# Performance work log

Hardware: AMD Instinct MI355X
Metric: run time of the kernel (lower is better)

Reference implementation:

```python
import jax, jax.numpy as jnp
import numpy as np

N_GRAPHS = 5000
NODES_PER_GRAPH = 100
EDGES_PER_GRAPH = 400
N_NODES = N_GRAPHS * NODES_PER_GRAPH
N_EDGES = N_GRAPHS * EDGES_PER_GRAPH
K = 2
DIMS = [74, 70, 65, 60, 55, 37]


def setup_inputs() -> dict:
    key = jax.random.key(0)
    ks = jax.random.split(key, 16)
    x = jax.random.normal(ks[0], (N_NODES, DIMS[0]), dtype=jnp.float32)
    # edges constrained within each graph: base node offset per graph + random local node
    edge_base = (jnp.arange(N_EDGES, dtype=jnp.int32) // EDGES_PER_GRAPH) * NODES_PER_GRAPH
    src = edge_base + jax.random.randint(ks[1], (N_EDGES,), 0, NODES_PER_GRAPH, dtype=jnp.int32)
    dst = edge_base + jax.random.randint(ks[2], (N_EDGES,), 0, NODES_PER_GRAPH, dtype=jnp.int32)
    graph_ids = (jnp.arange(N_NODES, dtype=jnp.int32) // NODES_PER_GRAPH)
    inp = {"x": x, "src": src, "dst": dst, "graph_ids": graph_ids}
    # TAGConv weights: Linear(in*(K+1) -> out) + bias, for each of 5 layers
    for i in range(5):
        fan_in = DIMS[i] * (K + 1)
        w = jax.random.normal(ks[3 + 2 * i], (fan_in, DIMS[i + 1]), dtype=jnp.float32) / np.sqrt(fan_in)
        b = jnp.zeros((DIMS[i + 1],), dtype=jnp.float32)
        inp[f"W{i}"] = w
        inp[f"b{i}"] = b
    inp["gate_w"] = jax.random.normal(ks[13], (DIMS[-1], 1), dtype=jnp.float32) / np.sqrt(DIMS[-1])
    inp["gate_b"] = jnp.zeros((1,), dtype=jnp.float32)
    return inp


def _forward(x, src, dst, graph_ids, Ws, bs, gate_w, gate_b):
    n = x.shape[0]
    # symmetric normalization with in-degree (DGL TAGConv convention), clamp min 1
    deg = jax.ops.segment_sum(jnp.ones_like(src, dtype=x.dtype), dst, num_segments=n)
    norm = jnp.clip(deg, 1.0, None) ** -0.5  # [N]
    norm = norm[:, None]

    def tagconv(h, W, b):
        feats = [h]
        cur = h
        for _ in range(K):
            msg = (cur * norm)[src]  # gather over edges
            cur = norm * jax.ops.segment_sum(msg, dst, num_segments=n)
            feats.append(cur)
        return jnp.concatenate(feats, axis=-1) @ W + b

    h = x
    for W, b in zip(Ws, bs):
        h = jax.nn.relu(tagconv(h, W, b))

    # GlobalAttentionPooling: per-graph softmax over gate scores, weighted sum
    gate = (h @ gate_w + gate_b)[:, 0]  # [N]
    gmax = jax.ops.segment_max(gate, graph_ids, num_segments=N_GRAPHS)
    e = jnp.exp(gate - gmax[graph_ids])
    z = jax.ops.segment_sum(e, graph_ids, num_segments=N_GRAPHS)
    alpha = e / z[graph_ids]
    pooled = jax.ops.segment_sum(h * alpha[:, None], graph_ids, num_segments=N_GRAPHS)  # [G, 37]
    return pooled.reshape(-1, 2, DIMS[-1])


def reference(x, src, dst, graph_ids, W0, b0, W1, b1, W2, b2, W3, b3, W4, b4, gate_w, gate_b):
    Ws = [W0, W1, W2, W3, W4]
    bs = [b0, b1, b2, b3, b4]
    return _forward(x, src, dst, graph_ids, Ws, bs, gate_w, gate_b)
```

## Files before the change

### kernel.cpp

```cpp
#include <hip/hip_runtime.h>
#include <math.h>


typedef __attribute__((ext_vector_type(8))) short bf16x8;
typedef __attribute__((ext_vector_type(4))) float f32x4;

constexpr int NODES  = 100;
constexpr int EDGES  = 400;
constexpr int STRIDE = 76;
constexpr int NTHR   = 512;

__device__ __align__(16) unsigned g_packW[86016];

struct __align__(16) Smem {
    float bufA[NODES * STRIDE];
    float bufB[NODES * STRIDE];
    float csr_val[EDGES];
    unsigned short csr_src[EDGES];
    int   row_start[NODES + 1];
    int   cntg[NODES];
    float nrm[NODES];
};

union FragU { unsigned u[4]; uint4 q; bf16x8 s; };

__device__ __forceinline__ void split_pair(float a, float b,
                                           unsigned& h, unsigned& l) {
    unsigned ua = __float_as_uint(a), ub = __float_as_uint(b);
    unsigned ha = ua & 0xFFFF0000u,  hb = ub & 0xFFFF0000u;
    h = (ua >> 16) | hb;
    float ra = a - __uint_as_float(ha);
    float rb = b - __uint_as_float(hb);
    l = (__float_as_uint(ra) >> 16) | (__float_as_uint(rb) & 0xFFFF0000u);
}

template<int D_IN, int D_OUT, int KT, int NT, int WOFF_U32>
__device__ __forceinline__ void repack_layer(const float* __restrict__ W, int idx) {
    constexpr int TILES = 3 * KT * NT;
    if (idx >= TILES * 64) return;
    int lane = idx & 63, tile = idx >> 6;
    int nt = tile % NT;
    int kt = (tile / NT) % KT;
    int b  = tile / (NT * KT);
    int col = nt * 16 + (lane & 15);
    int kg  = (lane >> 4) << 2;
    float v[8];
#pragma unroll
    for (int i = 0; i < 8; ++i) {
        int k = kt * 32 + ((i >= 4) ? 16 : 0) + kg + (i & 3);
        float f = 0.f;
        if (k < D_IN && col < D_OUT) f = W[(b * D_IN + k) * D_OUT + col];
        v[i] = f;
    }
    unsigned hu[4], lu[4];
#pragma unroll
    for (int p = 0; p < 4; ++p) split_pair(v[2*p], v[2*p+1], hu[p], lu[p]);
    unsigned* dst = g_packW + WOFF_U32 + (tile * 64 + lane) * 8;
    *(uint4*)(dst)     = make_uint4(hu[0], hu[1], hu[2], hu[3]);
    *(uint4*)(dst + 4) = make_uint4(lu[0], lu[1], lu[2], lu[3]);
}

__global__ void repack_kernel(const float* __restrict__ W0, const float* __restrict__ W1,
                              const float* __restrict__ W2, const float* __restrict__ W3,
                              const float* __restrict__ W4) {
    int idx = blockIdx.x * 256 + threadIdx.x;
    switch (blockIdx.y) {
    case 0: repack_layer<74, 70, 3, 5,     0>(W0, idx); break;
    case 1: repack_layer<70, 65, 3, 5, 23040>(W1, idx); break;
    case 2: repack_layer<65, 60, 3, 4, 46080>(W2, idx); break;
    case 3: repack_layer<60, 55, 2, 4, 64512>(W3, idx); break;
    case 4: repack_layer<55, 37, 2, 3, 76800>(W4, idx); break;
    }
}

template<int D_IN>
__device__ __forceinline__ void propagate(const float* __restrict__ in,
                                          float* __restrict__ outb,
                                          const unsigned short* __restrict__ csr_src,
                                          const float* __restrict__ csr_val,
                                          const int* __restrict__ row_start,
                                          const float* __restrict__ nrm,
                                          int wave, int lane)
{
    constexpr int CH = (D_IN + 3) / 4;
    constexpr int PR = (CH + 1) / 2;
    constexpr int T  = NODES * PR;
    constexpr int R4 = STRIDE / 4;
    const float4* __restrict__ in4 = (const float4*)in;
    float4* __restrict__ out4 = (float4*)outb;

    const int lo = (T * (6 * wave)) / 56;
    const int hi = (wave == 7) ? T : (T * (6 * (wave + 1))) / 56;

    for (int t = lo + lane; t < hi; t += 64) {
        int n = t / PR;
        int p = t - n * PR;
        int c0 = 2 * p;
        int c1 = c0 + 1;
        bool has2 = (c1 < CH);
        int c1r = has2 ? c1 : c0;
        int beg = row_start[n], end = row_start[n + 1];
        float ax0 = 0.f, ay0 = 0.f, az0 = 0.f, aw0 = 0.f;
        float ax1 = 0.f, ay1 = 0.f, az1 = 0.f, aw1 = 0.f;
        int e = beg;
        for (; e + 3 < end; e += 4) {
            int   s0 = csr_src[e],     s1 = csr_src[e + 1];
            int   s2 = csr_src[e + 2], s3 = csr_src[e + 3];
            float q0 = csr_val[e],     q1 = csr_val[e + 1];
            float q2 = csr_val[e + 2], q3 = csr_val[e + 3];
            const float4* r0 = in4 + s0 * R4;
            const float4* r1 = in4 + s1 * R4;
            const float4* r2 = in4 + s2 * R4;
            const float4* r3 = in4 + s3 * R4;
            float4 u0 = r0[c0], v0 = r0[c1r];
            float4 u1 = r1[c0], v1 = r1[c1r];
            float4 u2 = r2[c0], v2 = r2[c1r];
            float4 u3 = r3[c0], v3 = r3[c1r];
            ax0 = fmaf(q0, u0.x, ax0); ay0 = fmaf(q0, u0.y, ay0);
            az0 = fmaf(q0, u0.z, az0); aw0 = fmaf(q0, u0.w, aw0);
            ax1 = fmaf(q0, v0.x, ax1); ay1 = fmaf(q0, v0.y, ay1);
            az1 = fmaf(q0, v0.z, az1); aw1 = fmaf(q0, v0.w, aw1);
            ax0 = fmaf(q1, u1.x, ax0); ay0 = fmaf(q1, u1.y, ay0);
            az0 = fmaf(q1, u1.z, az0); aw0 = fmaf(q1, u1.w, aw0);
            ax1 = fmaf(q1, v1.x, ax1); ay1 = fmaf(q1, v1.y, ay1);
            az1 = fmaf(q1, v1.z, az1); aw1 = fmaf(q1, v1.w, aw1);
            ax0 = fmaf(q2, u2.x, ax0); ay0 = fmaf(q2, u2.y, ay0);
            az0 = fmaf(q2, u2.z, az0); aw0 = fmaf(q2, u2.w, aw0);
            ax1 = fmaf(q2, v2.x, ax1); ay1 = fmaf(q2, v2.y, ay1);
            az1 = fmaf(q2, v2.z, az1); aw1 = fmaf(q2, v2.w, aw1);
            ax0 = fmaf(q3, u3.x, ax0); ay0 = fmaf(q3, u3.y, ay0);
            az0 = fmaf(q3, u3.z, az0); aw0 = fmaf(q3, u3.w, aw0);
            ax1 = fmaf(q3, v3.x, ax1); ay1 = fmaf(q3, v3.y, ay1);
            az1 = fmaf(q3, v3.z, az1); aw1 = fmaf(q3, v3.w, aw1);
        }
        for (; e < end; ++e) {
            int s = csr_src[e];
            float q = csr_val[e];
            const float4* r = in4 + s * R4;
            float4 u = r[c0], v = r[c1r];
            ax0 = fmaf(q, u.x, ax0); ay0 = fmaf(q, u.y, ay0);
            az0 = fmaf(q, u.z, az0); aw0 = fmaf(q, u.w, aw0);
            ax1 = fmaf(q, v.x, ax1); ay1 = fmaf(q, v.y, ay1);
            az1 = fmaf(q, v.z, az1); aw1 = fmaf(q, v.w, aw1);
        }
        float sn = nrm[n];
        float4 o0 = { ax0 * sn, ay0 * sn, az0 * sn, aw0 * sn };
        out4[n * R4 + c0] = o0;
        if (has2) {
            float4 o1 = { ax1 * sn, ay1 * sn, az1 * sn, aw1 * sn };
            out4[n * R4 + c1] = o1;
        }
    }
}

template<int D_IN, int D_OUT, int KT, int NT, int WOFF_U32>
__device__ __forceinline__ void dense_block(const float* __restrict__ buf, int b,
                                            int mt, int lane, f32x4 (&acc)[NT]) {
    int row = mt * 16 + (lane & 15);
    row = row > NODES - 1 ? NODES - 1 : row;
    const float* __restrict__ hrow = buf + row * STRIDE;
    const int kg = (lane >> 4) << 2;
    const uint4* __restrict__ wb =
        (const uint4*)(g_packW + WOFF_U32) + b * (KT * NT * 128) + lane * 2;
#pragma unroll
    for (int kt = 0; kt < KT; ++kt) {
        int o0 = kt * 32 + kg;      if (o0 > 72) o0 = 72;
        int o1 = kt * 32 + 16 + kg; if (o1 > 72) o1 = 72;
        const float4 f0 = *(const float4*)(hrow + o0);
        const float4 f1 = *(const float4*)(hrow + o1);
        FragU Ah, Al;
        split_pair(f0.x, f0.y, Ah.u[0], Al.u[0]);
        split_pair(f0.z, f0.w, Ah.u[1], Al.u[1]);
        split_pair(f1.x, f1.y, Ah.u[2], Al.u[2]);
        split_pair(f1.z, f1.w, Ah.u[3], Al.u[3]);
#pragma unroll
        for (int nt = 0; nt < NT; ++nt) {
            const uint4* __restrict__ wl = wb + (kt * NT + nt) * 128;
            FragU Bh, Bl;
            Bh.q = wl[0];
            Bl.q = wl[1];
            acc[nt] = __builtin_amdgcn_mfma_f32_16x16x32_bf16(Ah.s, Bh.s, acc[nt], 0, 0, 0);
            acc[nt] = __builtin_amdgcn_mfma_f32_16x16x32_bf16(Ah.s, Bl.s, acc[nt], 0, 0, 0);
            acc[nt] = __builtin_amdgcn_mfma_f32_16x16x32_bf16(Al.s, Bh.s, acc[nt], 0, 0, 0);
        }
    }
}

template<int D_IN, int D_OUT, int KT, int NT, int WOFF_U32>
__device__ __forceinline__ void tag_layer(Smem& sm,
                                          float* __restrict__ S,
                                          float* __restrict__ T,
                                          const float* __restrict__ Bv,
                                          int tid)
{
    const int wave  = __builtin_amdgcn_readfirstlane(tid >> 6);
    const int lane  = tid & 63;
    const bool m_act = wave < 7;

    f32x4 acc[NT];
#pragma unroll
    for (int nt = 0; nt < NT; ++nt) acc[nt] = (f32x4)(0.f);

    if (m_act) dense_block<D_IN, D_OUT, KT, NT, WOFF_U32>(S, 0, wave, lane, acc);
    propagate<D_IN>(S, T, sm.csr_src, sm.csr_val, sm.row_start, sm.nrm, wave, lane);
    __syncthreads();
    if (m_act) dense_block<D_IN, D_OUT, KT, NT, WOFF_U32>(T, 1, wave, lane, acc);
    propagate<D_IN>(T, S, sm.csr_src, sm.csr_val, sm.row_start, sm.nrm, wave, lane);
    __syncthreads();
    if (m_act) {
        dense_block<D_IN, D_OUT, KT, NT, WOFF_U32>(S, 2, wave, lane, acc);
#pragma unroll
        for (int nt = 0; nt < NT; ++nt) {
            int col = nt * 16 + (lane & 15);
            if (col < D_OUT) {
                float bias = Bv[col];
#pragma unroll
                for (int r = 0; r < 4; ++r) {
                    int row = wave * 16 + ((lane >> 4) << 2) + r;
                    if (row < NODES)
                        T[row * STRIDE + col] = fmaxf(acc[nt][r] + bias, 0.f);
                }
            }
        }
    }
    __syncthreads();
}

__global__ __launch_bounds__(NTHR, 4)
void drug_graph_conv_kernel(
    const float* __restrict__ x,
    const int*   __restrict__ src,
    const int*   __restrict__ dst,
    const float* __restrict__ b0, const float* __restrict__ b1,
    const float* __restrict__ b2, const float* __restrict__ b3,
    const float* __restrict__ b4,
    const float* __restrict__ gate_w, const float* __restrict__ gate_b,
    float* __restrict__ out)
{
    __shared__ Smem sm;
    const int g     = blockIdx.x;
    const int tid   = threadIdx.x;
    const int nbase = g * NODES;

    {
        const float4* __restrict__ x4 = (const float4*)(x + (size_t)nbase * 74);
        for (int t = tid; t < NODES * 74 / 4; t += NTHR) {
            float4 v = x4[t];
            int idx = 4 * t;
#pragma unroll
            for (int k = 0; k < 4; ++k) {
                int ik = idx + k;
                int n  = ik / 74;
                int d  = ik - n * 74;
                float val = (k == 0) ? v.x : (k == 1) ? v.y : (k == 2) ? v.z : v.w;
                sm.bufA[n * STRIDE + d] = val;
            }
        }
    }
    for (int t = tid; t < NODES * 2; t += NTHR) {
        int n = t >> 1;
        sm.bufA[n * STRIDE + 74 + (t & 1)] = 0.f;
    }

    if (tid < NODES) sm.cntg[tid] = 0;
    __syncthreads();
    int es = 0, ed = 0;
    const bool ethr = tid < EDGES;
    if (ethr) {
        es = src[g * EDGES + tid] - nbase;
        ed = dst[g * EDGES + tid] - nbase;
        atomicAdd(&sm.cntg[ed], 1);
    }
    __syncthreads();

    if (tid < NODES) sm.nrm[tid] = rsqrtf((float)max(sm.cntg[tid], 1));
    if (tid < 64) {
        int v1 = (tid < NODES) ? sm.cntg[tid] : 0;
        int l2 = tid + 64;
        int v2 = (l2 < NODES) ? sm.cntg[l2] : 0;
        int s1 = v1;
#pragma unroll
        for (int d = 1; d < 64; d <<= 1) {
            int t2 = __shfl_up(s1, d, 64);
            if (tid >= d) s1 += t2;
        }
        int tot1 = __shfl(s1, 63, 64);
        int s2 = v2;
#pragma unroll
        for (int d = 1; d < 64; d <<= 1) {
            int t2 = __shfl_up(s2, d, 64);
            if (tid >= d) s2 += t2;
        }
        s2 += tot1;
        if (tid == 0) sm.row_start[0] = 0;
        sm.row_start[tid + 1] = s1;
        if (l2 < NODES) sm.row_start[l2 + 1] = s2;
    }
    __syncthreads();
    if (tid < NODES) sm.cntg[tid] = 0;
    __syncthreads();
    if (ethr) {
        int pos = atomicAdd(&sm.cntg[ed], 1);
        int slot = sm.row_start[ed] + pos;
        sm.csr_src[slot] = (unsigned short)es;
        sm.csr_val[slot] = sm.nrm[es];
    }
    __syncthreads();

    tag_layer<74, 70, 3, 5,     0>(sm, sm.bufA, sm.bufB, b0, tid);
    tag_layer<70, 65, 3, 5, 23040>(sm, sm.bufB, sm.bufA, b1, tid);
    tag_layer<65, 60, 3, 4, 46080>(sm, sm.bufA, sm.bufB, b2, tid);
    tag_layer<60, 55, 2, 4, 64512>(sm, sm.bufB, sm.bufA, b3, tid);
    tag_layer<55, 37, 2, 3, 76800>(sm, sm.bufA, sm.bufB, b4, tid);

    float* gate = (float*)sm.cntg;
    if (tid < NODES) {
        float s = gate_b[0];
#pragma unroll
        for (int k = 0; k < 37; ++k)
            s = fmaf(sm.bufB[tid * STRIDE + k], gate_w[k], s);
        gate[tid] = s;
    }
    __syncthreads();
    if (tid < 64) {
        float v1 = (tid < NODES) ? gate[tid] : -INFINITY;
        float v2 = (tid + 64 < NODES) ? gate[tid + 64] : -INFINITY;
        float m = fmaxf(v1, v2);
#pragma unroll
        for (int d = 32; d; d >>= 1) m = fmaxf(m, __shfl_xor(m, d, 64));
        float e1 = (tid < NODES) ? __expf(v1 - m) : 0.f;
        float e2 = (tid + 64 < NODES) ? __expf(v2 - m) : 0.f;
        float z = e1 + e2;
#pragma unroll
        for (int d = 32; d; d >>= 1) z += __shfl_xor(z, d, 64);
        float inv = 1.f / z;
        if (tid < NODES) gate[tid] = e1 * inv;
        if (tid + 64 < NODES) gate[tid + 64] = e2 * inv;
    }
    __syncthreads();

    {
        const int w = tid >> 6, l = tid & 63;
        if (l < 37) {
            float p = 0.f;
            for (int n = w; n < NODES; n += 8)
                p = fmaf(gate[n], sm.bufB[n * STRIDE + l], p);
            sm.csr_val[w * 37 + l] = p;
        }
    }
    __syncthreads();
    if (tid < 37) {
        float p = 0.f;
#pragma unroll
        for (int w = 0; w < 8; ++w) p += sm.csr_val[w * 37 + tid];
        out[g * 37 + tid] = p;
    }
}

extern "C" void kernel_launch(void* const* d_in, const int* in_sizes, int n_in,
                              void* d_out, int out_size, void* d_ws, size_t ws_size,
                              hipStream_t stream) {
    const float* x   = (const float*)d_in[0];
    const int*   src = (const int*)  d_in[1];
    const int*   dst = (const int*)  d_in[2];
    const float* W0 = (const float*)d_in[4];  const float* b0 = (const float*)d_in[5];
    const float* W1 = (const float*)d_in[6];  const float* b1 = (const float*)d_in[7];
    const float* W2 = (const float*)d_in[8];  const float* b2 = (const float*)d_in[9];
    const float* W3 = (const float*)d_in[10]; const float* b3 = (const float*)d_in[11];
    const float* W4 = (const float*)d_in[12]; const float* b4 = (const float*)d_in[13];
    const float* gw = (const float*)d_in[14]; const float* gb = (const float*)d_in[15];
    float* out = (float*)d_out;

    dim3 rg(12, 5, 1);
    repack_kernel<<<rg, 256, 0, stream>>>(W0, W1, W2, W3, W4);

    drug_graph_conv_kernel<<<5000, NTHR, 0, stream>>>(
        x, src, dst, b0, b1, b2, b3, b4, gw, gb, out);
}
```

Baseline: 807.9 us.

## Double block size to 1024 threads and split MFMA N-tiles across wave pairs

Raises the workgroup to 16 waves. The dense MFMA work is split so each pair of waves shares one 16-row M-tile, with each wave taking alternating N-tiles, which halves the per-wave accumulator count. Propagation work is redistributed unevenly: the 14 MFMA waves get a small share and the 2 non-MFMA waves take more. The aim is more latency hiding per block and fewer registers per wave. The risk is higher register pressure per CU under launch_bounds(1024, 8) and more contention at each barrier.

```diff
diff --git a/kernel.cpp b/kernel.cpp
--- a/kernel.cpp
+++ b/kernel.cpp
@@ -8,7 +8,7 @@
 constexpr int NODES  = 100;
 constexpr int EDGES  = 400;
 constexpr int STRIDE = 76;
-constexpr int NTHR   = 512;
+constexpr int NTHR   = 1024;
 
 __device__ __align__(16) unsigned g_packW[86016];
 
@@ -89,8 +89,11 @@
     const float4* __restrict__ in4 = (const float4*)in;
     float4* __restrict__ out4 = (float4*)outb;
 
-    const int lo = (T * (6 * wave)) / 56;
-    const int hi = (wave == 7) ? T : (T * (6 * (wave + 1))) / 56;
+    const int cw0 = (wave <= 14) ? 5 * wave : 70 + 15 * (wave - 14);
+    const int w1  = wave + 1;
+    const int cw1 = (w1 <= 14) ? 5 * w1 : 70 + 15 * (w1 - 14);
+    const int lo = (T * cw0) / 100;
+    const int hi = (T * cw1) / 100;
 
     for (int t = lo + lane; t < hi; t += 64) {
         int n = t / PR;
@@ -155,7 +158,9 @@
 
 template<int D_IN, int D_OUT, int KT, int NT, int WOFF_U32>
 __device__ __forceinline__ void dense_block(const float* __restrict__ buf, int b,
-                                            int mt, int lane, f32x4 (&acc)[NT]) {
+                                            int mt, int nh, int lane,
+                                            f32x4 (&acc)[(NT + 1) / 2]) {
+    constexpr int NTH = (NT + 1) / 2;
     int row = mt * 16 + (lane & 15);
     row = row > NODES - 1 ? NODES - 1 : row;
     const float* __restrict__ hrow = buf + row * STRIDE;
@@ -174,14 +179,17 @@
         split_pair(f1.x, f1.y, Ah.u[2], Al.u[2]);
         split_pair(f1.z, f1.w, Ah.u[3], Al.u[3]);
 #pragma unroll
-        for (int nt = 0; nt < NT; ++nt) {
-            const uint4* __restrict__ wl = wb + (kt * NT + nt) * 128;
-            FragU Bh, Bl;
-            Bh.q = wl[0];
-            Bl.q = wl[1];
-            acc[nt] = __builtin_amdgcn_mfma_f32_16x16x32_bf16(Ah.s, Bh.s, acc[nt], 0, 0, 0);
-            acc[nt] = __builtin_amdgcn_mfma_f32_16x16x32_bf16(Ah.s, Bl.s, acc[nt], 0, 0, 0);
-            acc[nt] = __builtin_amdgcn_mfma_f32_16x16x32_bf16(Al.s, Bh.s, acc[nt], 0, 0, 0);
+        for (int i = 0; i < NTH; ++i) {
+            int nt = nh + 2 * i;
+            if (nt < NT) {
+                const uint4* __restrict__ wl = wb + (kt * NT + nt) * 128;
+                FragU Bh, Bl;
+                Bh.q = wl[0];
+                Bl.q = wl[1];
+                acc[i] = __builtin_amdgcn_mfma_f32_16x16x32_bf16(Ah.s, Bh.s, acc[i], 0, 0, 0);
+                acc[i] = __builtin_amdgcn_mfma_f32_16x16x32_bf16(Ah.s, Bl.s, acc[i], 0, 0, 0);
+                acc[i] = __builtin_amdgcn_mfma_f32_16x16x32_bf16(Al.s, Bh.s, acc[i], 0, 0, 0);
+            }
         }
     }
 }
@@ -193,32 +201,38 @@
                                           const float* __restrict__ Bv,
                                           int tid)
 {
+    constexpr int NTH = (NT + 1) / 2;
     const int wave  = __builtin_amdgcn_readfirstlane(tid >> 6);
     const int lane  = tid & 63;
-    const bool m_act = wave < 7;
-
-    f32x4 acc[NT];
-#pragma unroll
-    for (int nt = 0; nt < NT; ++nt) acc[nt] = (f32x4)(0.f);
-
-    if (m_act) dense_block<D_IN, D_OUT, KT, NT, WOFF_U32>(S, 0, wave, lane, acc);
+    const int mt    = wave >> 1;
+    const int nh    = wave & 1;
+    const bool m_act = wave < 14;
+
+    f32x4 acc[NTH];
+#pragma unroll
+    for (int i = 0; i < NTH; ++i) acc[i] = (f32x4)(0.f);
+
+    if (m_act) dense_block<D_IN, D_OUT, KT, NT, WOFF_U32>(S, 0, mt, nh, lane, acc);
     propagate<D_IN>(S, T, sm.csr_src, sm.csr_val, sm.row_start, sm.nrm, wave, lane);
     __syncthreads();
-    if (m_act) dense_block<D_IN, D_OUT, KT, NT, WOFF_U32>(T, 1, wave, lane, acc);
+    if (m_act) dense_block<D_IN, D_OUT, KT, NT, WOFF_U32>(T, 1, mt, nh, lane, acc);
     propagate<D_IN>(T, S, sm.csr_src, sm.csr_val, sm.row_start, sm.nrm, wave, lane);
     __syncthreads();
     if (m_act) {
-        dense_block<D_IN, D_OUT, KT, NT, WOFF_U32>(S, 2, wave, lane, acc);
-#pragma unroll
-        for (int nt = 0; nt < NT; ++nt) {
-            int col = nt * 16 + (lane & 15);
-            if (col < D_OUT) {
-                float bias = Bv[col];
-#pragma unroll
-                for (int r = 0; r < 4; ++r) {
-                    int row = wave * 16 + ((lane >> 4) << 2) + r;
-                    if (row < NODES)
-                        T[row * STRIDE + col] = fmaxf(acc[nt][r] + bias, 0.f);
+        dense_block<D_IN, D_OUT, KT, NT, WOFF_U32>(S, 2, mt, nh, lane, acc);
+#pragma unroll
+        for (int i = 0; i < NTH; ++i) {
+            int nt = nh + 2 * i;
+            if (nt < NT) {
+                int col = nt * 16 + (lane & 15);
+                if (col < D_OUT) {
+                    float bias = Bv[col];
+#pragma unroll
+                    for (int r = 0; r < 4; ++r) {
+                        int row = mt * 16 + ((lane >> 4) << 2) + r;
+                        if (row < NODES)
+                            T[row * STRIDE + col] = fmaxf(acc[i][r] + bias, 0.f);
+                    }
                 }
             }
         }
@@ -226,7 +240,7 @@
     __syncthreads();
 }
 
-__global__ __launch_bounds__(NTHR, 4)
+__global__ __launch_bounds__(NTHR, 8)
 void drug_graph_conv_kernel(
     const float* __restrict__ x,
     const int*   __restrict__ src,
@@ -343,16 +357,16 @@
         const int w = tid >> 6, l = tid & 63;
         if (l < 37) {
             float p = 0.f;
-            for (int n = w; n < NODES; n += 8)
+            for (int n = w; n < NODES; n += 16)
                 p = fmaf(gate[n], sm.bufB[n * STRIDE + l], p);
-            sm.csr_val[w * 37 + l] = p;
+            sm.bufA[w * 37 + l] = p;
         }
     }
     __syncthreads();
     if (tid < 37) {
         float p = 0.f;
 #pragma unroll
-        for (int w = 0; w < 8; ++w) p += sm.csr_val[w * 37 + tid];
+        for (int w = 0; w < 16; ++w) p += sm.bufA[w * 37 + tid];
         out[g * 37 + tid] = p;
     }
 }
```

New measurement: 811.4 us. About the same (+0.4%).
